# Kernel tuning notes

Measured on AMD Instinct MI355X. Metric: run time of the kernel, lower is better.

Reference implementation:

```python
import jax, jax.numpy as jnp
import numpy as np

ALPHA = 0.15  # init kwarg alpha


def setup_inputs() -> dict:
    key = jax.random.key(0)
    k1, k2, k3, k4 = jax.random.split(key, 4)
    B, H, W, C = 16, 1024, 1024, 1
    I1 = jax.random.normal(k1, (B, H, W, C), jnp.float32)
    I2 = jax.random.normal(k2, (B, H, W, C), jnp.float32)
    u = jax.random.normal(k3, (B, H, W, C), jnp.float32)
    v = jax.random.normal(k4, (B, H, W, C), jnp.float32)
    return {"I1": I1, "I2": I2, "u": u, "v": v}


def _image_gradients(img):
    # Matches tf.image.image_gradients: returns (dy, dx), with last row/col zero.
    B, H, W, C = img.shape
    dy = jnp.concatenate([img[:, 1:, :, :] - img[:, :-1, :, :],
                          jnp.zeros((B, 1, W, C), img.dtype)], axis=1)
    dx = jnp.concatenate([img[:, :, 1:, :] - img[:, :, :-1, :],
                          jnp.zeros((B, H, 1, C), img.dtype)], axis=2)
    return dy, dx


def _warp(img, u, v):
    # Bilinear warp with zero padding at sample coords (x + 0.5*u, y + 0.5*v).
    # (The [-1,1] normalization + grid_sample align-corners denorm is identity.)
    B, H, W, C = img.shape
    x = jnp.arange(W, dtype=img.dtype)[None, None, :] + 0.5 * u[..., 0]  # (B,H,W)
    y = jnp.arange(H, dtype=img.dtype)[None, :, None] + 0.5 * v[..., 0]  # (B,H,W)
    x0 = jnp.floor(x)
    y0 = jnp.floor(y)
    x1 = x0 + 1.0
    y1 = y0 + 1.0
    wx1 = x - x0
    wx0 = 1.0 - wx1
    wy1 = y - y0
    wy0 = 1.0 - wy1
    img_flat = img.reshape(B, H * W, C)

    def gather(yi, xi):
        valid = (xi >= 0) & (xi <= W - 1) & (yi >= 0) & (yi <= H - 1)
        xi_c = jnp.clip(xi, 0, W - 1).astype(jnp.int32)
        yi_c = jnp.clip(yi, 0, H - 1).astype(jnp.int32)
        idx = (yi_c * W + xi_c).reshape(B, H * W, 1)
        vals = jnp.take_along_axis(img_flat, idx, axis=1).reshape(B, H, W, C)
        return vals * valid[..., None].astype(img.dtype)

    out = (gather(y0, x0) * (wy0 * wx0)[..., None]
           + gather(y0, x1) * (wy0 * wx1)[..., None]
           + gather(y1, x0) * (wy1 * wx0)[..., None]
           + gather(y1, x1) * (wy1 * wx1)[..., None])
    return out


def reference(I1, I2, u, v):
    # NOTE: faithful to the source, which assigns grad_x, grad_y = image_gradients(.)
    # even though tf.image.image_gradients returns (dy, dx).
    I1_grad_x, I1_grad_y = _image_gradients(I1)
    I1_warped = _warp(I1, u, v)
    dataTerm = I1_warped - I2
    u_next = u - ALPHA * dataTerm * I1_grad_x
    v_next = v - ALPHA * dataTerm * I1_grad_y
    return (u_next, v_next)
```

## Files before the change

kernel.cpp:

```cpp
#include <hip/hip_runtime.h>


#define ALPHA 0.15f
#define IMG_H 1024
#define IMG_W 1024
#define TW 128
#define TH 8
#define HALO 4
#define LW 140
#define LH 17
#define LDS_N 2560

typedef float f32x4 __attribute__((ext_vector_type(4)));

__global__ __launch_bounds__(256) void dataterm_kernel(
        const float* __restrict__ I1,
        const float* __restrict__ I2,
        const float* __restrict__ u,
        const float* __restrict__ v,
        float* __restrict__ out_u,
        float* __restrict__ out_v) {
    const int W = IMG_W, H = IMG_H;
    const int t   = threadIdx.x;
    const int tx0 = blockIdx.x * TW;
    const int ty0 = blockIdx.y * TH;
    const int b   = blockIdx.z;

    const float* __restrict__ I1b = I1 + (size_t)b * (size_t)(H * W);

    __shared__ float S[LDS_N];

    const int r  = t >> 5;
    const int cb = (t & 31) << 2;
    const int h  = ty0 + r;
    const int wb = tx0 + cb;
    const int p  = (b * H + h) * W + wb;

    f32x4 u4  = *(const f32x4*)(u + p);
    f32x4 v4  = *(const f32x4*)(v + p);
    f32x4 i24 = *(const f32x4*)(I2 + p);

    #pragma unroll
    for (int j = 0; j < 10; ++j) {
        int f  = t + 256 * j;
        int ly = f / LW;
        int lx = f - ly * LW;
        int gy = min(max(ty0 - HALO + min(ly, LH - 1), 0), H - 1);
        int gx = min(max(tx0 - HALO + lx, 0), W - 1);
        S[f] = I1b[gy * W + gx];
    }
    __syncthreads();

    const int cl = (HALO + r) * LW + HALO + cb;
    f32x4 c4 = *(const f32x4*)(S + cl);
    f32x4 d4 = *(const f32x4*)(S + cl + LW);
    float c4r = S[cl + 4];

    float gyv[4] = { d4.x - c4.x, d4.y - c4.y, d4.z - c4.z, d4.w - c4.w };
    float gxv[4] = { c4.y - c4.x, c4.z - c4.y, c4.w - c4.z, c4r - c4.w };

    float uu[4] = { u4.x, u4.y, u4.z, u4.w };
    float vv[4] = { v4.x, v4.y, v4.z, v4.w };
    float i2[4] = { i24.x, i24.y, i24.z, i24.w };
    float ru[4], rv[4];

    #pragma unroll
    for (int i = 0; i < 4; ++i) {
        float x = (float)(wb + i) + 0.5f * uu[i];
        float y = (float)h        + 0.5f * vv[i];

        float x0f = floorf(x);
        float y0f = floorf(y);
        float wx1 = x - x0f;
        float wx0 = 1.0f - wx1;
        float wy1 = y - y0f;
        float wy0 = 1.0f - wy1;

        int x0 = (int)x0f, y0 = (int)y0f;
        int x1 = x0 + 1,   y1 = y0 + 1;

        float vx0 = (x0 >= 0 && x0 <= W - 1) ? 1.0f : 0.0f;
        float vx1 = (x1 >= 0 && x1 <= W - 1) ? 1.0f : 0.0f;
        float vy0 = (y0 >= 0 && y0 <= H - 1) ? 1.0f : 0.0f;
        float vy1 = (y1 >= 0 && y1 <= H - 1) ? 1.0f : 0.0f;

        int lx0 = x0 - tx0 + HALO;
        int ly0 = y0 - ty0 + HALO;

        float g00, g01, g10, g11;
        if ((unsigned)lx0 <= (unsigned)(LW - 2) &&
            (unsigned)ly0 <= (unsigned)(LH - 2)) {
            int q = ly0 * LW + lx0;
            g00 = S[q]          * (vy0 * vx0);
            g01 = S[q + 1]      * (vy0 * vx1);
            g10 = S[q + LW]     * (vy1 * vx0);
            g11 = S[q + LW + 1] * (vy1 * vx1);
        } else {
            int x0c = min(max(x0, 0), W - 1);
            int x1c = min(max(x1, 0), W - 1);
            int y0c = min(max(y0, 0), H - 1);
            int y1c = min(max(y1, 0), H - 1);
            g00 = I1b[y0c * W + x0c] * (vy0 * vx0);
            g01 = I1b[y0c * W + x1c] * (vy0 * vx1);
            g10 = I1b[y1c * W + x0c] * (vy1 * vx0);
            g11 = I1b[y1c * W + x1c] * (vy1 * vx1);
        }

        float warped = g00 * (wy0 * wx0)
                     + g01 * (wy0 * wx1)
                     + g10 * (wy1 * wx0)
                     + g11 * (wy1 * wx1);

        float dataTerm = warped - i2[i];
        ru[i] = uu[i] - ALPHA * dataTerm * gyv[i];
        rv[i] = vv[i] - ALPHA * dataTerm * gxv[i];
    }

    f32x4 ruv = { ru[0], ru[1], ru[2], ru[3] };
    f32x4 rvv = { rv[0], rv[1], rv[2], rv[3] };
    __builtin_nontemporal_store(ruv, (f32x4*)(out_u + p));
    __builtin_nontemporal_store(rvv, (f32x4*)(out_v + p));
}

extern "C" void kernel_launch(void* const* d_in, const int* in_sizes, int n_in,
                              void* d_out, int out_size, void* d_ws, size_t ws_size,
                              hipStream_t stream) {
    const float* I1 = (const float*)d_in[0];
    const float* I2 = (const float*)d_in[1];
    const float* u  = (const float*)d_in[2];
    const float* v  = (const float*)d_in[3];

    int total = in_sizes[0];
    float* out_u = (float*)d_out;
    float* out_v = (float*)d_out + total;

    dim3 grid(IMG_W / TW, IMG_H / TH, total / (IMG_H * IMG_W));
    dataterm_kernel<<<grid, dim3(256), 0, stream>>>(I1, I2, u, v, out_u, out_v);
}
```

Measured before the change: 65.78 us.

## Stream vertical strips through an LDS ring buffer with register-staged prefetch

Each block now processes 8 consecutive 8-row strips instead of one. I1 rows are held in a 32-row circular LDS buffer, so halo rows are reused across strips instead of reloaded. The next strip's I1 rows and u/v/I2 vectors are prefetched into registers while the current strip computes. This cuts the redundant halo traffic (17 rows loaded per 8 output rows) and overlaps loads with compute, at the cost of 8x fewer blocks, more registers and a per-strip barrier.

Result: slower. 70.46 us (+7.1%).

```diff
diff --git a/kernel.cpp b/kernel.cpp
--- a/kernel.cpp
+++ b/kernel.cpp
@@ -5,11 +5,11 @@
 #define IMG_H 1024
 #define IMG_W 1024
 #define TW 128
-#define TH 8
 #define HALO 4
 #define LW 140
 #define LH 17
-#define LDS_N 2560
+#define RING 32
+#define STRIPS 8
 
 typedef float f32x4 __attribute__((ext_vector_type(4)));
 
@@ -23,103 +23,152 @@
     const int W = IMG_W, H = IMG_H;
     const int t   = threadIdx.x;
     const int tx0 = blockIdx.x * TW;
-    const int ty0 = blockIdx.y * TH;
+    const int sy0 = blockIdx.y * (STRIPS * 8);
     const int b   = blockIdx.z;
 
     const float* __restrict__ I1b = I1 + (size_t)b * (size_t)(H * W);
 
-    __shared__ float S[LDS_N];
+    __shared__ float S[RING * LW];
 
     const int r  = t >> 5;
     const int cb = (t & 31) << 2;
-    const int h  = ty0 + r;
     const int wb = tx0 + cb;
-    const int p  = (b * H + h) * W + wb;
 
+    int p = (b * H + (sy0 + r)) * W + wb;
     f32x4 u4  = *(const f32x4*)(u + p);
     f32x4 v4  = *(const f32x4*)(v + p);
     f32x4 i24 = *(const f32x4*)(I2 + p);
 
     #pragma unroll
     for (int j = 0; j < 10; ++j) {
-        int f  = t + 256 * j;
-        int ly = f / LW;
-        int lx = f - ly * LW;
-        int gy = min(max(ty0 - HALO + min(ly, LH - 1), 0), H - 1);
-        int gx = min(max(tx0 - HALO + lx, 0), W - 1);
-        S[f] = I1b[gy * W + gx];
+        int f = t + 256 * j;
+        if (f < LH * LW) {
+            int ly = f / LW;
+            int lx = f - ly * LW;
+            int rp = sy0 - 4 + ly;
+            int gy = min(max(rp, 0), H - 1);
+            int gx = min(max(tx0 - HALO + lx, 0), W - 1);
+            S[(rp & (RING - 1)) * LW + lx] = I1b[gy * W + gx];
+        }
     }
     __syncthreads();
 
-    const int cl = (HALO + r) * LW + HALO + cb;
-    f32x4 c4 = *(const f32x4*)(S + cl);
-    f32x4 d4 = *(const f32x4*)(S + cl + LW);
-    float c4r = S[cl + 4];
+    for (int it = 0; it < STRIPS; ++it) {
+        const int sy = sy0 + it * 8;
+        const int h  = sy + r;
+        const bool last = (it == STRIPS - 1);
 
-    float gyv[4] = { d4.x - c4.x, d4.y - c4.y, d4.z - c4.z, d4.w - c4.w };
-    float gxv[4] = { c4.y - c4.x, c4.z - c4.y, c4.w - c4.z, c4r - c4.w };
-
-    float uu[4] = { u4.x, u4.y, u4.z, u4.w };
-    float vv[4] = { v4.x, v4.y, v4.z, v4.w };
-    float i2[4] = { i24.x, i24.y, i24.z, i24.w };
-    float ru[4], rv[4];
-
-    #pragma unroll
-    for (int i = 0; i < 4; ++i) {
-        float x = (float)(wb + i) + 0.5f * uu[i];
-        float y = (float)h        + 0.5f * vv[i];
-
-        float x0f = floorf(x);
-        float y0f = floorf(y);
-        float wx1 = x - x0f;
-        float wx0 = 1.0f - wx1;
-        float wy1 = y - y0f;
-        float wy0 = 1.0f - wy1;
-
-        int x0 = (int)x0f, y0 = (int)y0f;
-        int x1 = x0 + 1,   y1 = y0 + 1;
-
-        float vx0 = (x0 >= 0 && x0 <= W - 1) ? 1.0f : 0.0f;
-        float vx1 = (x1 >= 0 && x1 <= W - 1) ? 1.0f : 0.0f;
-        float vy0 = (y0 >= 0 && y0 <= H - 1) ? 1.0f : 0.0f;
-        float vy1 = (y1 >= 0 && y1 <= H - 1) ? 1.0f : 0.0f;
-
-        int lx0 = x0 - tx0 + HALO;
-        int ly0 = y0 - ty0 + HALO;
-
-        float g00, g01, g10, g11;
-        if ((unsigned)lx0 <= (unsigned)(LW - 2) &&
-            (unsigned)ly0 <= (unsigned)(LH - 2)) {
-            int q = ly0 * LW + lx0;
-            g00 = S[q]          * (vy0 * vx0);
-            g01 = S[q + 1]      * (vy0 * vx1);
-            g10 = S[q + LW]     * (vy1 * vx0);
-            g11 = S[q + LW + 1] * (vy1 * vx1);
-        } else {
-            int x0c = min(max(x0, 0), W - 1);
-            int x1c = min(max(x1, 0), W - 1);
-            int y0c = min(max(y0, 0), H - 1);
-            int y1c = min(max(y1, 0), H - 1);
-            g00 = I1b[y0c * W + x0c] * (vy0 * vx0);
-            g01 = I1b[y0c * W + x1c] * (vy0 * vx1);
-            g10 = I1b[y1c * W + x0c] * (vy1 * vx0);
-            g11 = I1b[y1c * W + x1c] * (vy1 * vx1);
+        float stg[5];
+        f32x4 u4n = {}, v4n = {}, i2n = {};
+        if (!last) {
+            #pragma unroll
+            for (int j = 0; j < 5; ++j) {
+                int f = t + 256 * j;
+                if (f < 8 * LW) {
+                    int lyp = f / LW;
+                    int lx  = f - lyp * LW;
+                    int rp  = sy + 13 + lyp;
+                    int gy  = min(rp, H - 1);
+                    int gx  = min(max(tx0 - HALO + lx, 0), W - 1);
+                    stg[j] = I1b[gy * W + gx];
+                }
+            }
+            int pn = p + 8 * W;
+            u4n = *(const f32x4*)(u + pn);
+            v4n = *(const f32x4*)(v + pn);
+            i2n = *(const f32x4*)(I2 + pn);
         }
 
-        float warped = g00 * (wy0 * wx0)
-                     + g01 * (wy0 * wx1)
-                     + g10 * (wy1 * wx0)
-                     + g11 * (wy1 * wx1);
+        const int slc = (h & (RING - 1)) * LW + HALO + cb;
+        const int sld = ((h + 1) & (RING - 1)) * LW + HALO + cb;
+        f32x4 c4 = *(const f32x4*)(S + slc);
+        f32x4 d4 = *(const f32x4*)(S + sld);
+        float c4r = S[slc + 4];
 
-        float dataTerm = warped - i2[i];
-        ru[i] = uu[i] - ALPHA * dataTerm * gyv[i];
-        rv[i] = vv[i] - ALPHA * dataTerm * gxv[i];
+        float gyv[4] = { d4.x - c4.x, d4.y - c4.y, d4.z - c4.z, d4.w - c4.w };
+        float gxv[4] = { c4.y - c4.x, c4.z - c4.y, c4.w - c4.z, c4r - c4.w };
+
+        float uu[4] = { u4.x, u4.y, u4.z, u4.w };
+        float vv[4] = { v4.x, v4.y, v4.z, v4.w };
+        float i2[4] = { i24.x, i24.y, i24.z, i24.w };
+        float ru[4], rv[4];
+
+        #pragma unroll
+        for (int i = 0; i < 4; ++i) {
+            float x = (float)(wb + i) + 0.5f * uu[i];
+            float y = (float)h        + 0.5f * vv[i];
+
+            float x0f = floorf(x);
+            float y0f = floorf(y);
+            float wx1 = x - x0f;
+            float wx0 = 1.0f - wx1;
+            float wy1 = y - y0f;
+            float wy0 = 1.0f - wy1;
+
+            int x0 = (int)x0f, y0 = (int)y0f;
+            int x1 = x0 + 1,   y1 = y0 + 1;
+
+            float vx0 = (x0 >= 0 && x0 <= W - 1) ? 1.0f : 0.0f;
+            float vx1 = (x1 >= 0 && x1 <= W - 1) ? 1.0f : 0.0f;
+            float vy0 = (y0 >= 0 && y0 <= H - 1) ? 1.0f : 0.0f;
+            float vy1 = (y1 >= 0 && y1 <= H - 1) ? 1.0f : 0.0f;
+
+            int lx0 = x0 - tx0 + HALO;
+            int lyw = y0 - (sy - 4);
+
+            float g00, g01, g10, g11;
+            if ((unsigned)lx0 <= (unsigned)(LW - 2) &&
+                (unsigned)lyw <= (unsigned)(LH - 2)) {
+                int q0 = (y0 & (RING - 1)) * LW + lx0;
+                int q1 = (y1 & (RING - 1)) * LW + lx0;
+                g00 = S[q0]     * (vy0 * vx0);
+                g01 = S[q0 + 1] * (vy0 * vx1);
+                g10 = S[q1]     * (vy1 * vx0);
+                g11 = S[q1 + 1] * (vy1 * vx1);
+            } else {
+                int x0c = min(max(x0, 0), W - 1);
+                int x1c = min(max(x1, 0), W - 1);
+                int y0c = min(max(y0, 0), H - 1);
+                int y1c = min(max(y1, 0), H - 1);
+                g00 = I1b[y0c * W + x0c] * (vy0 * vx0);
+                g01 = I1b[y0c * W + x1c] * (vy0 * vx1);
+                g10 = I1b[y1c * W + x0c] * (vy1 * vx0);
+                g11 = I1b[y1c * W + x1c] * (vy1 * vx1);
+            }
+
+            float warped = g00 * (wy0 * wx0)
+                         + g01 * (wy0 * wx1)
+                         + g10 * (wy1 * wx0)
+                         + g11 * (wy1 * wx1);
+
+            float dataTerm = warped - i2[i];
+            ru[i] = uu[i] - ALPHA * dataTerm * gyv[i];
+            rv[i] = vv[i] - ALPHA * dataTerm * gxv[i];
+        }
+
+        f32x4 ruv = { ru[0], ru[1], ru[2], ru[3] };
+        f32x4 rvv = { rv[0], rv[1], rv[2], rv[3] };
+        __builtin_nontemporal_store(ruv, (f32x4*)(out_u + p));
+        __builtin_nontemporal_store(rvv, (f32x4*)(out_v + p));
+
+        if (!last) {
+            #pragma unroll
+            for (int j = 0; j < 5; ++j) {
+                int f = t + 256 * j;
+                if (f < 8 * LW) {
+                    int lyp = f / LW;
+                    int lx  = f - lyp * LW;
+                    int rp  = sy + 13 + lyp;
+                    S[(rp & (RING - 1)) * LW + lx] = stg[j];
+                }
+            }
+        }
+
+        __syncthreads();
+
+        u4 = u4n; v4 = v4n; i24 = i2n;
+        p += 8 * W;
     }
-
-    f32x4 ruv = { ru[0], ru[1], ru[2], ru[3] };
-    f32x4 rvv = { rv[0], rv[1], rv[2], rv[3] };
-    __builtin_nontemporal_store(ruv, (f32x4*)(out_u + p));
-    __builtin_nontemporal_store(rvv, (f32x4*)(out_v + p));
 }
 
 extern "C" void kernel_launch(void* const* d_in, const int* in_sizes, int n_in,
@@ -134,6 +183,6 @@
     float* out_u = (float*)d_out;
     float* out_v = (float*)d_out + total;
 
-    dim3 grid(IMG_W / TW, IMG_H / TH, total / (IMG_H * IMG_W));
+    dim3 grid(IMG_W / TW, IMG_H / (STRIPS * 8), total / (IMG_H * IMG_W));
     dataterm_kernel<<<grid, dim3(256), 0, stream>>>(I1, I2, u, v, out_u, out_v);
 }
```
